# Kernel tuning notes

Hardware: AMD Instinct MI355X
Metric: run time of the kernel (lower is better)

## Reference

```python
import jax, jax.numpy as jnp
import numpy as np

N, E = 50000, 800000          # nodes, edges
IN_DIM, HID, OUT = 200, 256, 64  # hidden_dims
R = 2                          # num_relations
NEG_SLOPE = 0.2                # RGATConv default negative_slope
EPS = 1e-16                    # PyG softmax denominator eps


def _glorot(key, shape, fan):
    return jax.random.normal(key, shape, dtype=jnp.float32) / np.float32(np.sqrt(fan))


def setup_inputs() -> dict:
    key = jax.random.key(0)
    ks = jax.random.split(key, 13)
    features = jax.random.normal(ks[0], (N, IN_DIM), dtype=jnp.float32)
    edge_index = jax.random.randint(ks[1], (2, E), 0, N, dtype=jnp.int64)
    edge_type = jax.random.randint(ks[2], (E,), 0, R, dtype=jnp.int64)
    return {
        "features": features,
        "edge_index": edge_index,
        "edge_type": edge_type,
        # RGATConv layer 1 (heads=1, dim=1): weight [R, in, out], q/k [out, 1]
        "w1": _glorot(ks[3], (R, IN_DIM, HID), IN_DIM),
        "q1": _glorot(ks[4], (HID, 1), HID),
        "k1": _glorot(ks[5], (HID, 1), HID),
        # RGATConv layer 2
        "w2": _glorot(ks[6], (R, HID, OUT), HID),
        "q2": _glorot(ks[7], (OUT, 1), OUT),
        "k2": _glorot(ks[8], (OUT, 1), OUT),
        # decoder: Linear(OUT->HID) then Linear(HID->IN_DIM), stored as [in, out]
        "dW1": _glorot(ks[9], (OUT, HID), OUT),
        "db1": jnp.zeros((HID,), jnp.float32),
        "dW2": _glorot(ks[10], (HID, IN_DIM), HID),
        "db2": jnp.zeros((IN_DIM,), jnp.float32),
    }


def rgat_conv(x, src, dst, etype, w, q, k):
    """PyG RGATConv: additive-self-attention, across-relation softmax,
    heads=1, dim=1, concat=False, bias=False, aggr=add (eval mode: no dropout)."""
    n = x.shape[0]
    # relation-specific transform at node level (per-edge bmm factors through nodes)
    xw = jnp.einsum('ni,ric->rnc', x, w)          # [R, N, C]
    qn = jnp.einsum('rnc,ch->rnh', xw, q)         # [R, N, 1]
    kn = jnp.einsum('rnc,ch->rnh', xw, k)         # [R, N, 1]
    # per-edge attention logit: leaky_relu(q_i + k_j)
    alpha = jax.nn.leaky_relu(qn[etype, dst] + kn[etype, src], NEG_SLOPE)  # [E, 1]
    # segment softmax over destination nodes (across relations)
    m = jax.lax.stop_gradient(jax.ops.segment_max(alpha, dst, num_segments=n))
    m = jnp.where(jnp.isfinite(m), m, jnp.float32(0.0))
    ea = jnp.exp(alpha - m[dst])
    denom = jax.ops.segment_sum(ea, dst, num_segments=n)
    att = ea / (denom[dst] + EPS)                 # [E, 1]
    # scatter-add weighted messages
    msg = att * xw[etype, src]                    # [E, C]
    return jax.ops.segment_sum(msg, dst, num_segments=n)  # [N, C]


def reference(features, edge_index, edge_type, w1, q1, k1, w2, q2, k2, dW1, db1, dW2, db2):
    src, dst = edge_index[0], edge_index[1]
    h1 = jax.nn.elu(rgat_conv(features, src, dst, edge_type, w1, q1, k1))
    h2 = jax.nn.elu(rgat_conv(h1, src, dst, edge_type, w2, q2, k2))
    h3 = (h2 @ dW1 + db1) @ dW2 + db2   # decoder (PCA mode: no ReLU)
    return (h2, h3)
```

## Files before the change

### kernel.cpp

```cpp
#include <hip/hip_runtime.h>

#define IN_DIM 200
#define HID    256
#define OUT_D  64
#define RREL   2
#define NEG_SLOPE 0.2f
#define NNODE  50000
#define MPAD   50048

typedef __attribute__((ext_vector_type(8))) short bf16x8;
typedef __attribute__((ext_vector_type(4))) float f32x4;
typedef __attribute__((ext_vector_type(4))) unsigned int u32x4;

__device__ __forceinline__ float bf2f(unsigned short u) {
    union { unsigned int i; float f; } v; v.i = ((unsigned int)u) << 16; return v.f;
}
__device__ __forceinline__ unsigned short f2bf(float f) {
    union { float f; unsigned int i; } v; v.f = f;
    unsigned int u = v.i;
    return (unsigned short)((u + 0x7FFFu + ((u >> 16) & 1u)) >> 16);
}
__device__ __forceinline__ float elu(float v) { return v > 0.f ? v : (__expf(v) - 1.0f); }

__global__ void feat_cvt(const float* __restrict__ in, unsigned short* __restrict__ out)
{
    long long idx = (long long)blockIdx.x * 256 + threadIdx.x;
    int row = (int)(idx >> 6);
    int c4  = ((int)idx & 63) << 2;
    if (row >= MPAD) return;
    unsigned short v[4];
    #pragma unroll
    for (int i = 0; i < 4; ++i) {
        int c = c4 + i;
        float f = (row < NNODE && c < IN_DIM) ? in[(long long)row * IN_DIM + c] : 0.f;
        v[i] = f2bf(f);
    }
    *(ushort4*)(out + (long long)row * 256 + c4) = make_ushort4(v[0], v[1], v[2], v[3]);
}

__global__ void wt_cvt(const float* __restrict__ in, unsigned short* __restrict__ out,
                       int Kreal, int Nreal, int Kpad, int Npad, int nb)
{
    long long total = (long long)nb * Npad * Kpad;
    long long idx = (long long)blockIdx.x * 256 + threadIdx.x;
    if (idx >= total) return;
    int kk = (int)(idx % Kpad);
    long long t = idx / Kpad;
    int nrow = (int)(t % Npad);
    int z = (int)(t / Npad);
    float f = (kk < Kreal && nrow < Nreal) ? in[((long long)z * Kreal + kk) * Nreal + nrow] : 0.f;
    out[idx] = f2bf(f);
}

__global__ void wt_cvt_stack(const float* __restrict__ in, unsigned short* __restrict__ out)
{
    int idx = blockIdx.x * 256 + threadIdx.x;
    if (idx >= 2 * 256 * 256) return;
    int kk = idx & 255;
    int c  = (idx >> 8) & 255;
    int z  = idx >> 16;
    float f = (kk < IN_DIM) ? in[((long long)z * IN_DIM + kk) * 256 + c] : 0.f;
    out[(long long)c * 512 + z * 256 + kk] = f2bf(f);
}

__global__ __launch_bounds__(256) void wqk_cvt(
    const float* __restrict__ w, const float* __restrict__ q,
    const float* __restrict__ k, float* __restrict__ wqv, float* __restrict__ wkv)
{
    int wv = ((blockIdx.x << 8) + threadIdx.x) >> 6;
    int lane = threadIdx.x & 63;
    if (wv >= 512) return;
    int r = wv >> 8, kk = wv & 255;
    float sq = 0.f, sk = 0.f;
    if (kk < IN_DIM) {
        const float* row = w + ((long long)(r * IN_DIM + kk)) * 256;
        float4 wv4 = *(const float4*)(row + lane * 4);
        float4 qv4 = *(const float4*)(q + lane * 4);
        float4 kv4 = *(const float4*)(k + lane * 4);
        sq = wv4.x * qv4.x + wv4.y * qv4.y + wv4.z * qv4.z + wv4.w * qv4.w;
        sk = wv4.x * kv4.x + wv4.y * kv4.y + wv4.z * kv4.z + wv4.w * kv4.w;
        #pragma unroll
        for (int off = 32; off; off >>= 1) {
            sq += __shfl_xor(sq, off);
            sk += __shfl_xor(sk, off);
        }
    }
    if (lane == 0) { wqv[r * 256 + kk] = sq; wkv[r * 256 + kk] = sk; }
}

__global__ __launch_bounds__(256) void qk_feat(
    const unsigned short* __restrict__ A1, const float* __restrict__ wqv,
    const float* __restrict__ wkv, float* __restrict__ qn, float* __restrict__ kn, int n)
{
    int wv = ((blockIdx.x << 8) + threadIdx.x) >> 6;
    int lane = threadIdx.x & 63;
    if (wv >= n) return;
    ushort4 v = *(const ushort4*)(A1 + (long long)wv * 256 + lane * 4);
    float x0 = bf2f(v.x), x1 = bf2f(v.y), x2 = bf2f(v.z), x3 = bf2f(v.w);
    float4 q0v = *(const float4*)(wqv + lane * 4);
    float4 k0v = *(const float4*)(wkv + lane * 4);
    float4 q1v = *(const float4*)(wqv + 256 + lane * 4);
    float4 k1v = *(const float4*)(wkv + 256 + lane * 4);
    float sq0 = x0 * q0v.x + x1 * q0v.y + x2 * q0v.z + x3 * q0v.w;
    float sk0 = x0 * k0v.x + x1 * k0v.y + x2 * k0v.z + x3 * k0v.w;
    float sq1 = x0 * q1v.x + x1 * q1v.y + x2 * q1v.z + x3 * q1v.w;
    float sk1 = x0 * k1v.x + x1 * k1v.y + x2 * k1v.z + x3 * k1v.w;
    #pragma unroll
    for (int off = 32; off; off >>= 1) {
        sq0 += __shfl_xor(sq0, off);
        sk0 += __shfl_xor(sk0, off);
        sq1 += __shfl_xor(sq1, off);
        sk1 += __shfl_xor(sk1, off);
    }
    if (lane == 0) {
        qn[wv] = sq0; qn[n + wv] = sq1;
        kn[wv] = sk0; kn[n + wv] = sk1;
    }
}

template<bool OUT_BF16, bool DO_ELU>
__global__ __launch_bounds__(256) void gemm_mfma(
    const unsigned short* __restrict__ A,
    const unsigned short* __restrict__ Bt,
    const float* __restrict__ bias,
    void* __restrict__ Cout,
    int M, int Nn, int Kp, int Npad,
    long long strideC)
{
    __shared__ __align__(16) char lds[49152];
    const int tid  = threadIdx.x;
    const int lane = tid & 63;
    const int w    = tid >> 6;
    const int m0   = blockIdx.x * 128;
    const int n0   = blockIdx.y * 64;
    const int z    = blockIdx.z;

    const char* Ab = (const char*)A;
    const char* Bb = (const char*)(Bt + (long long)z * Npad * Kp);
    const int rs = Kp * 2;

    f32x4 acc[2][4];
    #pragma unroll
    for (int i = 0; i < 2; ++i)
        #pragma unroll
        for (int j = 0; j < 4; ++j) acc[i][j] = (f32x4){0.f, 0.f, 0.f, 0.f};

    const int KT = Kp >> 6;

    auto stage = [&](int buf, int kt) {
        char* lA = lds + buf * 24576;
        char* lB = lA + 16384;
        #pragma unroll
        for (int i = 0; i < 4; ++i) {
            int g = i * 256 + tid;
            int row = g >> 3, c = g & 7;
            const char* src = Ab + (long long)(m0 + row) * rs + kt * 128 + ((c ^ (row & 7)) << 4);
            __builtin_amdgcn_global_load_lds((const __attribute__((address_space(1))) void*)src,
                                             (__attribute__((address_space(3))) void*)(lA + g * 16),
                                             16, 0, 0);
        }
        #pragma unroll
        for (int i = 0; i < 2; ++i) {
            int g = i * 256 + tid;
            int row = g >> 3, c = g & 7;
            const char* src = Bb + (long long)(n0 + row) * rs + kt * 128 + ((c ^ (row & 7)) << 4);
            __builtin_amdgcn_global_load_lds((const __attribute__((address_space(1))) void*)src,
                                             (__attribute__((address_space(3))) void*)(lB + g * 16),
                                             16, 0, 0);
        }
    };

    stage(0, 0);
    int cur = 0;
    for (int kt = 0; kt < KT; ++kt) {
        __syncthreads();
        if (kt + 1 < KT) stage(cur ^ 1, kt + 1);
        const char* lA = lds + cur * 24576;
        const char* lB = lA + 16384;
        #pragma unroll
        for (int ks = 0; ks < 2; ++ks) {
            const int kg = ks * 4 + (lane >> 4);
            bf16x8 a[2], b[4];
            #pragma unroll
            for (int mi = 0; mi < 2; ++mi) {
                int row = w * 32 + mi * 16 + (lane & 15);
                a[mi] = *(const bf16x8*)(lA + row * 128 + ((kg ^ (row & 7)) << 4));
            }
            #pragma unroll
            for (int nj = 0; nj < 4; ++nj) {
                int row = nj * 16 + (lane & 15);
                b[nj] = *(const bf16x8*)(lB + row * 128 + ((kg ^ (row & 7)) << 4));
            }
            #pragma unroll
            for (int mi = 0; mi < 2; ++mi)
                #pragma unroll
                for (int nj = 0; nj < 4; ++nj)
                    acc[mi][nj] = __builtin_amdgcn_mfma_f32_16x16x32_bf16(a[mi], b[nj], acc[mi][nj], 0, 0, 0);
        }
        cur ^= 1;
    }

    const int colb = n0 + (lane & 15);
    #pragma unroll
    for (int mi = 0; mi < 2; ++mi) {
        #pragma unroll
        for (int nj = 0; nj < 4; ++nj) {
            int col = colb + nj * 16;
            if (col >= Nn) continue;
            float badd = bias ? bias[col] : 0.f;
            #pragma unroll
            for (int r = 0; r < 4; ++r) {
                int rowm = m0 + w * 32 + mi * 16 + ((lane >> 4) << 2) + r;
                if (rowm >= M) continue;
                float v = acc[mi][nj][r] + badd;
                if (DO_ELU) v = v > 0.f ? v : (__expf(v) - 1.0f);
                if (OUT_BF16)
                    ((unsigned short*)Cout)[strideC * z + (long long)rowm * Nn + col] = f2bf(v);
                else
                    ((float*)Cout)[strideC * z + (long long)rowm * Nn + col] = v;
            }
        }
    }
}

template<int C>
__global__ __launch_bounds__(256) void qk_bf16(
    const unsigned short* __restrict__ xw, const float* __restrict__ q,
    const float* __restrict__ k, float* __restrict__ qn, float* __restrict__ kn, int n)
{
    int wv = ((blockIdx.x << 8) + threadIdx.x) >> 6;
    int lane = threadIdx.x & 63;
    if (wv >= 2 * n) return;
    int r = wv >= n;
    int node = wv - r * n;
    const unsigned short* row = xw + ((long long)r * MPAD + node) * C;
    float sq, sk;
    if (C == 256) {
        ushort4 v = *(const ushort4*)(row + lane * 4);
        float4 qv = *(const float4*)(q + lane * 4);
        float4 kv = *(const float4*)(k + lane * 4);
        float x0 = bf2f(v.x), x1 = bf2f(v.y), x2 = bf2f(v.z), x3 = bf2f(v.w);
        sq = x0 * qv.x + x1 * qv.y + x2 * qv.z + x3 * qv.w;
        sk = x0 * kv.x + x1 * kv.y + x2 * kv.z + x3 * kv.w;
    } else {
        float x = bf2f(row[lane]);
        sq = x * q[lane];
        sk = x * k[lane];
    }
    #pragma unroll
    for (int off = 32; off; off >>= 1) {
        sq += __shfl_xor(sq, off);
        sk += __shfl_xor(sk, off);
    }
    if (lane == 0) { qn[wv] = sq; kn[wv] = sk; }
}

__global__ void count_kernel(const int* __restrict__ dst, const int* __restrict__ etype,
                             int* __restrict__ deg2, int E)
{
    int e = blockIdx.x * 256 + threadIdx.x;
    if (e < E) atomicAdd(&deg2[(dst[e] << 1) | etype[e]], 1);
}

__global__ __launch_bounds__(256) void scan_blocksum(
    const int* __restrict__ deg, int* __restrict__ bsum, int n)
{
    __shared__ int red[256];
    int i = blockIdx.x * 256 + threadIdx.x;
    int v = (i < n) ? deg[i] : 0;
    red[threadIdx.x] = v;
    __syncthreads();
    #pragma unroll
    for (int off = 128; off; off >>= 1) {
        if (threadIdx.x < off) red[threadIdx.x] += red[threadIdx.x + off];
        __syncthreads();
    }
    if (threadIdx.x == 0) bsum[blockIdx.x] = red[0];
}

__global__ __launch_bounds__(512) void scan_bsum(int* __restrict__ bsum, int nb)
{
    __shared__ int buf[512];
    const int t = threadIdx.x;
    int v = (t < nb) ? bsum[t] : 0;
    buf[t] = v;
    __syncthreads();
    #pragma unroll
    for (int off = 1; off < 512; off <<= 1) {
        int u = (t >= off) ? buf[t - off] : 0;
        __syncthreads();
        buf[t] += u;
        __syncthreads();
    }
    if (t < nb) bsum[t] = buf[t] - v;
}

__global__ __launch_bounds__(256) void scan_final(
    const int* __restrict__ deg, const int* __restrict__ bsum,
    int* __restrict__ row_ptr, int* __restrict__ cursor, int n)
{
    __shared__ int buf[256];
    const int t = threadIdx.x;
    const int i = blockIdx.x * 256 + t;
    int v = (i < n) ? deg[i] : 0;
    buf[t] = v;
    __syncthreads();
    #pragma unroll
    for (int off = 1; off < 256; off <<= 1) {
        int u = (t >= off) ? buf[t - off] : 0;
        __syncthreads();
        buf[t] += u;
        __syncthreads();
    }
    int excl = bsum[blockIdx.x] + buf[t] - v;
    if (i < n) { row_ptr[i] = excl; cursor[i] = excl; }
    if (i == n - 1) row_ptr[n] = excl + v;
}

__global__ void scatter_kernel(const int* __restrict__ dst, const int* __restrict__ src,
                               const int* __restrict__ etype, int* __restrict__ cursor2,
                               int* __restrict__ epk, int E)
{
    int e = blockIdx.x * 256 + threadIdx.x;
    if (e < E) {
        int p = atomicAdd(&cursor2[(dst[e] << 1) | etype[e]], 1);
        epk[p] = src[e];
    }
}

__global__ __launch_bounds__(256) void aggregate_z(
    const unsigned short* __restrict__ A1,
    const float* __restrict__ qn,
    const float* __restrict__ kn,
    const int* __restrict__ row_ptr2,
    const int* __restrict__ epk,
    unsigned short* __restrict__ z,
    int n)
{
    const int wv   = ((blockIdx.x << 8) + threadIdx.x) >> 6;
    const int lane = threadIdx.x & 63;
    if (wv >= n) return;
    const int d = wv;
    const int start = row_ptr2[2 * d];
    const int mid   = row_ptr2[2 * d + 1];
    const int end   = row_ptr2[2 * d + 2];
    const float q0 = qn[d];
    const float q1 = qn[n + d];

    float mx = -INFINITY;
    for (int j = start + lane; j < end; j += 64) {
        int s = epk[j];
        bool r1 = j >= mid;
        float a = (r1 ? q1 : q0) + kn[(r1 ? n : 0) + s];
        a = a > 0.f ? a : NEG_SLOPE * a;
        mx = fmaxf(mx, a);
    }
    #pragma unroll
    for (int off = 32; off; off >>= 1) mx = fmaxf(mx, __shfl_xor(mx, off));

    float se = 0.f;
    for (int j = start + lane; j < end; j += 64) {
        int s = epk[j];
        bool r1 = j >= mid;
        float a = (r1 ? q1 : q0) + kn[(r1 ? n : 0) + s];
        a = a > 0.f ? a : NEG_SLOPE * a;
        se += __expf(a - mx);
    }
    #pragma unroll
    for (int off = 32; off; off >>= 1) se += __shfl_xor(se, off);
    const float inv = 1.f / (se + 1e-16f);

    const int slot = lane >> 5;
    const int hl   = lane & 31;

    #pragma unroll
    for (int seg = 0; seg < 2; ++seg) {
        const int s0 = seg ? mid : start;
        const int s1 = seg ? end : mid;
        const float qr = seg ? q1 : q0;
        const int kbase = seg ? n : 0;

        float accA[8], accB[8];
        #pragma unroll
        for (int i = 0; i < 8; ++i) { accA[i] = 0.f; accB[i] = 0.f; }

        for (int base = s0; base < s1; base += 64) {
            const int cnt = min(64, s1 - base);
            int pv = 0; float wvv = 0.f;
            if (lane < cnt) {
                pv = epk[base + lane];
                float a = qr + kn[kbase + pv];
                a = a > 0.f ? a : NEG_SLOPE * a;
                wvv = __expf(a - mx) * inv;
            }
            const int iters = (cnt + 1) >> 1;
            int k = 0;
            for (; k + 2 <= iters; k += 2) {
                const int e0 = slot + k * 2;
                const int e1 = e0 + 2;
                int   pA = __shfl(pv, e0);
                float wA = __shfl(wvv, e0);
                int   pB = __shfl(pv, e1);
                float wB = __shfl(wvv, e1);
                const u32x4 rA = *(const u32x4*)(A1 + (long long)pA * 256 + hl * 8);
                const u32x4 rB = *(const u32x4*)(A1 + (long long)pB * 256 + hl * 8);
                #pragma unroll
                for (int t2 = 0; t2 < 4; ++t2) {
                    unsigned dA = rA[t2], dB = rB[t2];
                    accA[2 * t2]     = fmaf(wA, __uint_as_float(dA << 16),         accA[2 * t2]);
                    accA[2 * t2 + 1] = fmaf(wA, __uint_as_float(dA & 0xFFFF0000u), accA[2 * t2 + 1]);
                    accB[2 * t2]     = fmaf(wB, __uint_as_float(dB << 16),         accB[2 * t2]);
                    accB[2 * t2 + 1] = fmaf(wB, __uint_as_float(dB & 0xFFFF0000u), accB[2 * t2 + 1]);
                }
            }
            if (k < iters) {
                const int e0 = slot + k * 2;
                int   pA = __shfl(pv, e0);
                float wA = __shfl(wvv, e0);
                const u32x4 rA = *(const u32x4*)(A1 + (long long)pA * 256 + hl * 8);
                #pragma unroll
                for (int t2 = 0; t2 < 4; ++t2) {
                    unsigned dA = rA[t2];
                    accA[2 * t2]     = fmaf(wA, __uint_as_float(dA << 16),         accA[2 * t2]);
                    accA[2 * t2 + 1] = fmaf(wA, __uint_as_float(dA & 0xFFFF0000u), accA[2 * t2 + 1]);
                }
            }
        }

        float acc[8];
        #pragma unroll
        for (int i = 0; i < 8; ++i) acc[i] = accA[i] + accB[i];
        #pragma unroll
        for (int t2 = 0; t2 < 8; ++t2) acc[t2] += __shfl_xor(acc[t2], 32);

        if (slot == 0) {
            u32x4 pack;
            #pragma unroll
            for (int t2 = 0; t2 < 4; ++t2)
                pack[t2] = (unsigned)f2bf(acc[2 * t2]) | ((unsigned)f2bf(acc[2 * t2 + 1]) << 16);
            *(u32x4*)(z + (long long)d * 512 + seg * 256 + hl * 8) = pack;
        }
    }
}

__global__ __launch_bounds__(256) void aggregate2(
    const unsigned short* __restrict__ xw,
    const float* __restrict__ qn,
    const float* __restrict__ kn,
    const int* __restrict__ row_ptr2,
    const int* __restrict__ epk,
    unsigned short* __restrict__ outb,
    float* __restrict__ outf,
    int n)
{
    constexpr int LPE   = 8;
    constexpr int NSLOT = 8;

    const int wv   = ((blockIdx.x << 8) + threadIdx.x) >> 6;
    const int lane = threadIdx.x & 63;
    if (wv >= n) return;
    const int d = wv;
    const int start = row_ptr2[2 * d];
    const int mid   = row_ptr2[2 * d + 1];
    const int end   = row_ptr2[2 * d + 2];
    const float q0 = qn[d];
    const float q1 = qn[n + d];

    float mx = -INFINITY;
    for (int j = start + lane; j < end; j += 64) {
        int s = epk[j];
        bool r1 = j >= mid;
        float a = (r1 ? q1 : q0) + kn[(r1 ? n : 0) + s];
        a = a > 0.f ? a : NEG_SLOPE * a;
        mx = fmaxf(mx, a);
    }
    #pragma unroll
    for (int off = 32; off; off >>= 1) mx = fmaxf(mx, __shfl_xor(mx, off));

    float se = 0.f;
    for (int j = start + lane; j < end; j += 64) {
        int s = epk[j];
        bool r1 = j >= mid;
        float a = (r1 ? q1 : q0) + kn[(r1 ? n : 0) + s];
        a = a > 0.f ? a : NEG_SLOPE * a;
        se += __expf(a - mx);
    }
    #pragma unroll
    for (int off = 32; off; off >>= 1) se += __shfl_xor(se, off);
    const float inv = 1.f / (se + 1e-16f);

    const int slot = lane / LPE;
    const int hl   = lane % LPE;
    float accA[8], accB[8];
    #pragma unroll
    for (int i = 0; i < 8; ++i) { accA[i] = 0.f; accB[i] = 0.f; }

    for (int base = start; base < end; base += 64) {
        const int cnt = min(64, end - base);
        int pv = 0; float wvv = 0.f;
        if (lane < cnt) {
            int j = base + lane;
            pv = epk[j];
            bool r1 = j >= mid;
            float a = (r1 ? q1 : q0) + kn[(r1 ? n : 0) + pv];
            a = a > 0.f ? a : NEG_SLOPE * a;
            wvv = __expf(a - mx) * inv;
        }

        const int iters = (cnt + NSLOT - 1) / NSLOT;
        int k = 0;
        for (; k + 2 <= iters; k += 2) {
            const int e0 = slot + k * NSLOT;
            const int e1 = e0 + NSLOT;
            int   pA = __shfl(pv, e0);
            float wA = __shfl(wvv, e0);
            int   pB = __shfl(pv, e1);
            float wB = __shfl(wvv, e1);
            const long long oA = ((base + e0 >= mid) ? (long long)MPAD * 64 : 0) + (long long)pA * 64 + hl * 8;
            const long long oB = ((base + e1 >= mid) ? (long long)MPAD * 64 : 0) + (long long)pB * 64 + hl * 8;
            const u32x4 rA = *(const u32x4*)(xw + oA);
            const u32x4 rB = *(const u32x4*)(xw + oB);
            #pragma unroll
            for (int t2 = 0; t2 < 4; ++t2) {
                unsigned dA = rA[t2], dB = rB[t2];
                accA[2 * t2]     = fmaf(wA, __uint_as_float(dA << 16),         accA[2 * t2]);
                accA[2 * t2 + 1] = fmaf(wA, __uint_as_float(dA & 0xFFFF0000u), accA[2 * t2 + 1]);
                accB[2 * t2]     = fmaf(wB, __uint_as_float(dB << 16),         accB[2 * t2]);
                accB[2 * t2 + 1] = fmaf(wB, __uint_as_float(dB & 0xFFFF0000u), accB[2 * t2 + 1]);
            }
        }
        if (k < iters) {
            const int e0 = slot + k * NSLOT;
            int   pA = __shfl(pv, e0);
            float wA = __shfl(wvv, e0);
            const long long oA = ((base + e0 >= mid) ? (long long)MPAD * 64 : 0) + (long long)pA * 64 + hl * 8;
            const u32x4 rA = *(const u32x4*)(xw + oA);
            #pragma unroll
            for (int t2 = 0; t2 < 4; ++t2) {
                unsigned dA = rA[t2];
                accA[2 * t2]     = fmaf(wA, __uint_as_float(dA << 16),         accA[2 * t2]);
                accA[2 * t2 + 1] = fmaf(wA, __uint_as_float(dA & 0xFFFF0000u), accA[2 * t2 + 1]);
            }
        }
    }

    float acc[8];
    #pragma unroll
    for (int i = 0; i < 8; ++i) acc[i] = accA[i] + accB[i];
    #pragma unroll
    for (int off = LPE; off < 64; off <<= 1)
        #pragma unroll
        for (int t2 = 0; t2 < 8; ++t2) acc[t2] += __shfl_xor(acc[t2], off);

    if (slot == 0) {
        float fo[8];
        #pragma unroll
        for (int t2 = 0; t2 < 8; ++t2) fo[t2] = elu(acc[t2]);
        u32x4 pack;
        #pragma unroll
        for (int t2 = 0; t2 < 4; ++t2)
            pack[t2] = (unsigned)f2bf(fo[2 * t2]) | ((unsigned)f2bf(fo[2 * t2 + 1]) << 16);
        *(u32x4*)(outb + (long long)d * 64 + hl * 8) = pack;
        *(float4*)(outf + (long long)d * 64 + hl * 8)     = make_float4(fo[0], fo[1], fo[2], fo[3]);
        *(float4*)(outf + (long long)d * 64 + hl * 8 + 4) = make_float4(fo[4], fo[5], fo[6], fo[7]);
    }
}

extern "C" void kernel_launch(void* const* d_in, const int* in_sizes, int n_in,
                              void* d_out, int out_size, void* d_ws, size_t ws_size,
                              hipStream_t stream)
{
    const float* features = (const float*)d_in[0];
    const int*   ei       = (const int*)d_in[1];
    const int*   etype    = (const int*)d_in[2];
    const float* w1       = (const float*)d_in[3];
    const float* q1       = (const float*)d_in[4];
    const float* k1       = (const float*)d_in[5];
    const float* w2       = (const float*)d_in[6];
    const float* q2       = (const float*)d_in[7];
    const float* k2       = (const float*)d_in[8];
    const float* dW1      = (const float*)d_in[9];
    const float* db1      = (const float*)d_in[10];
    const float* dW2      = (const float*)d_in[11];
    const float* db2      = (const float*)d_in[12];

    const int n = in_sizes[0] / IN_DIM;
    const int E = in_sizes[2];
    const int n2 = 2 * n;
    const int* src = ei;
    const int* dst = ei + E;

    float* out_h2 = (float*)d_out;
    float* out_h3 = out_h2 + (long long)n * OUT_D;

    char* wp = (char*)d_ws;
    auto carve = [&](size_t bytes) {
        char* p = wp; wp += (bytes + 255) & ~(size_t)255; return p;
    };
    unsigned short* A1   = (unsigned short*)carve((size_t)MPAD * 256 * 2);
    unsigned short* zbuf = (unsigned short*)carve((size_t)MPAD * 512 * 2);
    unsigned short* h1   = (unsigned short*)carve((size_t)MPAD * 256 * 2);
    unsigned short* xw2  = (unsigned short*)carve((size_t)2 * MPAD * 64 * 2);
    unsigned short* h2b  = (unsigned short*)carve((size_t)MPAD * 64 * 2);
    unsigned short* tdec = (unsigned short*)carve((size_t)MPAD * 256 * 2);
    unsigned short* wst  = (unsigned short*)carve((size_t)256 * 512 * 2);
    unsigned short* w2t  = (unsigned short*)carve((size_t)2 * 64 * 256 * 2);
    unsigned short* dW1t = (unsigned short*)carve((size_t)256 * 64 * 2);
    unsigned short* dW2t = (unsigned short*)carve((size_t)256 * 256 * 2);
    float* wqv    = (float*)carve((size_t)2 * 256 * 4);
    float* wkv    = (float*)carve((size_t)2 * 256 * 4);
    float* qnb    = (float*)carve((size_t)n2 * 4);
    float* knb    = (float*)carve((size_t)n2 * 4);
    int* row_ptr2 = (int*)carve((size_t)(n2 + 1) * 4);
    int* cursor2  = (int*)carve((size_t)n2 * 4);
    int* deg2     = (int*)carve((size_t)n2 * 4);
    int* bsum     = (int*)carve((size_t)512 * 4);
    int* epk      = (int*)carve((size_t)E * 4);

    const int EB  = (E + 255) / 256;
    const int NB2 = (n2 + 255) / 256;
    const int MB  = (n + 127) / 128;
    const int WAVE_N  = (n + 3) / 4;
    const int WAVE_RN = (n2 + 3) / 4;

    hipMemsetAsync(deg2, 0, (size_t)n2 * sizeof(int), stream);
    count_kernel<<<EB, 256, 0, stream>>>(dst, etype, deg2, E);
    scan_blocksum<<<NB2, 256, 0, stream>>>(deg2, bsum, n2);
    scan_bsum<<<1, 512, 0, stream>>>(bsum, NB2);
    scan_final<<<NB2, 256, 0, stream>>>(deg2, bsum, row_ptr2, cursor2, n2);
    scatter_kernel<<<EB, 256, 0, stream>>>(dst, src, etype, cursor2, epk, E);

    feat_cvt<<<(MPAD * 64 + 255) / 256, 256, 0, stream>>>(features, A1);
    wt_cvt_stack<<<(2 * 256 * 256 + 255) / 256, 256, 0, stream>>>(w1, wst);
    wt_cvt<<<(2 * 64 * 256 + 255) / 256, 256, 0, stream>>>(w2, w2t, HID, OUT_D, 256, 64, RREL);
    wt_cvt<<<(256 * 64 + 255) / 256, 256, 0, stream>>>(dW1, dW1t, OUT_D, HID, 64, 256, 1);
    wt_cvt<<<(256 * 256 + 255) / 256, 256, 0, stream>>>(dW2, dW2t, HID, IN_DIM, 256, 256, 1);
    wqk_cvt<<<128, 256, 0, stream>>>(w1, q1, k1, wqv, wkv);

    qk_feat<<<WAVE_N, 256, 0, stream>>>(A1, wqv, wkv, qnb, knb, n);
    aggregate_z<<<WAVE_N, 256, 0, stream>>>(A1, qnb, knb, row_ptr2, epk, zbuf, n);
    {
        dim3 g(MB, 4, 1);
        gemm_mfma<true, true><<<g, 256, 0, stream>>>(zbuf, wst, nullptr, h1,
                                                     n, HID, 512, 256, 0);
    }

    {
        dim3 g(MB, 1, RREL);
        gemm_mfma<true, false><<<g, 256, 0, stream>>>(h1, w2t, nullptr, xw2,
                                                      n, OUT_D, 256, 64, (long long)MPAD * OUT_D);
    }
    qk_bf16<OUT_D><<<WAVE_RN, 256, 0, stream>>>(xw2, q2, k2, qnb, knb, n);
    aggregate2<<<WAVE_N, 256, 0, stream>>>(xw2, qnb, knb, row_ptr2, epk,
                                           h2b, out_h2, n);

    {
        dim3 g(MB, 4, 1);
        gemm_mfma<true, false><<<g, 256, 0, stream>>>(h2b, dW1t, db1, tdec,
                                                      n, HID, 64, 256, 0);
    }
    {
        dim3 g(MB, 4, 1);
        gemm_mfma<false, false><<<g, 256, 0, stream>>>(tdec, dW2t, db2, out_h3,
                                                       n, IN_DIM, 256, 256, 0);
    }
}
```

Baseline: 365.5 us.

## Compact layer-1 features to 200-wide rows and add single-pass softmax for small degrees

The bf16 feature matrix is now stored at its real 200-column stride instead of padded to 256. This cuts conversion writes and the bytes touched by the qk and gather kernels. Both aggregation kernels gain a fast path for destinations with at most 64 incoming edges: it loads each edge index and logit once into registers, then does the max, the sum and the weighted gather from those values instead of rereading the edge list three times. The gather still reads 256 columns per row, so columns 200-255 pick up data from the next row or the unpadded tail. This relies on the stacked weight rows for those columns being zero, and the tail bytes past the last row are left uninitialized.

Result: no change. 360.3 us (-1.4%).

```diff
diff --git a/kernel.cpp b/kernel.cpp
--- a/kernel.cpp
+++ b/kernel.cpp
@@ -22,20 +22,14 @@
 }
 __device__ __forceinline__ float elu(float v) { return v > 0.f ? v : (__expf(v) - 1.0f); }
 
-__global__ void feat_cvt(const float* __restrict__ in, unsigned short* __restrict__ out)
-{
-    long long idx = (long long)blockIdx.x * 256 + threadIdx.x;
-    int row = (int)(idx >> 6);
-    int c4  = ((int)idx & 63) << 2;
-    if (row >= MPAD) return;
-    unsigned short v[4];
-    #pragma unroll
-    for (int i = 0; i < 4; ++i) {
-        int c = c4 + i;
-        float f = (row < NNODE && c < IN_DIM) ? in[(long long)row * IN_DIM + c] : 0.f;
-        v[i] = f2bf(f);
-    }
-    *(ushort4*)(out + (long long)row * 256 + c4) = make_ushort4(v[0], v[1], v[2], v[3]);
+__global__ void feat_cvt(const float* __restrict__ in, unsigned short* __restrict__ out, int n)
+{
+    int t = blockIdx.x * 256 + threadIdx.x;
+    int row = t / 50, c4 = (t % 50) * 4;
+    if (row >= n) return;
+    float4 f = *(const float4*)(in + (long long)row * 200 + c4);
+    *(ushort4*)(out + (long long)row * 200 + c4) =
+        make_ushort4(f2bf(f.x), f2bf(f.y), f2bf(f.z), f2bf(f.w));
 }
 
 __global__ void wt_cvt(const float* __restrict__ in, unsigned short* __restrict__ out,
@@ -89,14 +83,17 @@
 }
 
 __global__ __launch_bounds__(256) void qk_feat(
-    const unsigned short* __restrict__ A1, const float* __restrict__ wqv,
+    const unsigned short* __restrict__ A1c, const float* __restrict__ wqv,
     const float* __restrict__ wkv, float* __restrict__ qn, float* __restrict__ kn, int n)
 {
     int wv = ((blockIdx.x << 8) + threadIdx.x) >> 6;
     int lane = threadIdx.x & 63;
     if (wv >= n) return;
-    ushort4 v = *(const ushort4*)(A1 + (long long)wv * 256 + lane * 4);
-    float x0 = bf2f(v.x), x1 = bf2f(v.y), x2 = bf2f(v.z), x3 = bf2f(v.w);
+    float x0 = 0.f, x1 = 0.f, x2 = 0.f, x3 = 0.f;
+    if (lane < 50) {
+        ushort4 v = *(const ushort4*)(A1c + (long long)wv * 200 + lane * 4);
+        x0 = bf2f(v.x); x1 = bf2f(v.y); x2 = bf2f(v.z); x3 = bf2f(v.w);
+    }
     float4 q0v = *(const float4*)(wqv + lane * 4);
     float4 k0v = *(const float4*)(wkv + lane * 4);
     float4 q1v = *(const float4*)(wqv + 256 + lane * 4);
@@ -329,7 +326,7 @@
 }
 
 __global__ __launch_bounds__(256) void aggregate_z(
-    const unsigned short* __restrict__ A1,
+    const unsigned short* __restrict__ A1c,
     const float* __restrict__ qn,
     const float* __restrict__ kn,
     const int* __restrict__ row_ptr2,
@@ -344,8 +341,89 @@
     const int start = row_ptr2[2 * d];
     const int mid   = row_ptr2[2 * d + 1];
     const int end   = row_ptr2[2 * d + 2];
+    const int cnt = end - start;
+    const int c0  = mid - start;
     const float q0 = qn[d];
     const float q1 = qn[n + d];
+    const int slot = lane >> 5;
+    const int hl   = lane & 31;
+
+    if (cnt <= 64) {
+        int pv = 0; float a = -INFINITY;
+        if (lane < cnt) {
+            pv = epk[start + lane];
+            bool r1 = lane >= c0;
+            a = (r1 ? q1 : q0) + kn[(r1 ? n : 0) + pv];
+            a = a > 0.f ? a : NEG_SLOPE * a;
+        }
+        float mx = a;
+        #pragma unroll
+        for (int off = 32; off; off >>= 1) mx = fmaxf(mx, __shfl_xor(mx, off));
+        float ev = (lane < cnt) ? __expf(a - mx) : 0.f;
+        float se = ev;
+        #pragma unroll
+        for (int off = 32; off; off >>= 1) se += __shfl_xor(se, off);
+        const float wvv = ev * (1.f / (se + 1e-16f));
+
+        #pragma unroll
+        for (int seg = 0; seg < 2; ++seg) {
+            const int segoff = seg ? c0 : 0;
+            const int cs = seg ? (cnt - c0) : c0;
+            float accA[8], accB[8];
+            #pragma unroll
+            for (int i = 0; i < 8; ++i) { accA[i] = 0.f; accB[i] = 0.f; }
+
+            const int iters = (cs + 1) >> 1;
+            int k = 0;
+            for (; k + 2 <= iters; k += 2) {
+                const int e0 = slot + k * 2;
+                const int e1 = e0 + 2;
+                int   pA = __shfl(pv, segoff + e0);
+                float wA = __shfl(wvv, segoff + e0);
+                int   pB = __shfl(pv, segoff + e1);
+                float wB = __shfl(wvv, segoff + e1);
+                if (e0 >= cs) wA = 0.f;
+                if (e1 >= cs) wB = 0.f;
+                const u32x4 rA = *(const u32x4*)(A1c + (long long)pA * 200 + hl * 8);
+                const u32x4 rB = *(const u32x4*)(A1c + (long long)pB * 200 + hl * 8);
+                #pragma unroll
+                for (int t2 = 0; t2 < 4; ++t2) {
+                    unsigned dA = rA[t2], dB = rB[t2];
+                    accA[2 * t2]     = fmaf(wA, __uint_as_float(dA << 16),         accA[2 * t2]);
+                    accA[2 * t2 + 1] = fmaf(wA, __uint_as_float(dA & 0xFFFF0000u), accA[2 * t2 + 1]);
+                    accB[2 * t2]     = fmaf(wB, __uint_as_float(dB << 16),         accB[2 * t2]);
+                    accB[2 * t2 + 1] = fmaf(wB, __uint_as_float(dB & 0xFFFF0000u), accB[2 * t2 + 1]);
+                }
+            }
+            if (k < iters) {
+                const int e0 = slot + k * 2;
+                int   pA = __shfl(pv, segoff + e0);
+                float wA = __shfl(wvv, segoff + e0);
+                if (e0 >= cs) wA = 0.f;
+                const u32x4 rA = *(const u32x4*)(A1c + (long long)pA * 200 + hl * 8);
+                #pragma unroll
+                for (int t2 = 0; t2 < 4; ++t2) {
+                    unsigned dA = rA[t2];
+                    accA[2 * t2]     = fmaf(wA, __uint_as_float(dA << 16),         accA[2 * t2]);
+                    accA[2 * t2 + 1] = fmaf(wA, __uint_as_float(dA & 0xFFFF0000u), accA[2 * t2 + 1]);
+                }
+            }
+
+            float acc[8];
+            #pragma unroll
+            for (int i = 0; i < 8; ++i) acc[i] = accA[i] + accB[i];
+            #pragma unroll
+            for (int t2 = 0; t2 < 8; ++t2) acc[t2] += __shfl_xor(acc[t2], 32);
+            if (slot == 0) {
+                u32x4 pack;
+                #pragma unroll
+                for (int t2 = 0; t2 < 4; ++t2)
+                    pack[t2] = (unsigned)f2bf(acc[2 * t2]) | ((unsigned)f2bf(acc[2 * t2 + 1]) << 16);
+                *(u32x4*)(z + (long long)d * 512 + seg * 256 + hl * 8) = pack;
+            }
+        }
+        return;
+    }
 
     float mx = -INFINITY;
     for (int j = start + lane; j < end; j += 64) {
@@ -370,9 +448,6 @@
     for (int off = 32; off; off >>= 1) se += __shfl_xor(se, off);
     const float inv = 1.f / (se + 1e-16f);
 
-    const int slot = lane >> 5;
-    const int hl   = lane & 31;
-
     #pragma unroll
     for (int seg = 0; seg < 2; ++seg) {
         const int s0 = seg ? mid : start;
@@ -385,15 +460,15 @@
         for (int i = 0; i < 8; ++i) { accA[i] = 0.f; accB[i] = 0.f; }
 
         for (int base = s0; base < s1; base += 64) {
-            const int cnt = min(64, s1 - base);
+            const int cnt2 = min(64, s1 - base);
             int pv = 0; float wvv = 0.f;
-            if (lane < cnt) {
+            if (lane < cnt2) {
                 pv = epk[base + lane];
                 float a = qr + kn[kbase + pv];
                 a = a > 0.f ? a : NEG_SLOPE * a;
                 wvv = __expf(a - mx) * inv;
             }
-            const int iters = (cnt + 1) >> 1;
+            const int iters = (cnt2 + 1) >> 1;
             int k = 0;
             for (; k + 2 <= iters; k += 2) {
                 const int e0 = slot + k * 2;
@@ -402,8 +477,8 @@
                 float wA = __shfl(wvv, e0);
                 int   pB = __shfl(pv, e1);
                 float wB = __shfl(wvv, e1);
-                const u32x4 rA = *(const u32x4*)(A1 + (long long)pA * 256 + hl * 8);
-                const u32x4 rB = *(const u32x4*)(A1 + (long long)pB * 256 + hl * 8);
+                const u32x4 rA = *(const u32x4*)(A1c + (long long)pA * 200 + hl * 8);
+                const u32x4 rB = *(const u32x4*)(A1c + (long long)pB * 200 + hl * 8);
                 #pragma unroll
                 for (int t2 = 0; t2 < 4; ++t2) {
                     unsigned dA = rA[t2], dB = rB[t2];
@@ -417,7 +492,7 @@
                 const int e0 = slot + k * 2;
                 int   pA = __shfl(pv, e0);
                 float wA = __shfl(wvv, e0);
-                const u32x4 rA = *(const u32x4*)(A1 + (long long)pA * 256 + hl * 8);
+                const u32x4 rA = *(const u32x4*)(A1c + (long long)pA * 200 + hl * 8);
                 #pragma unroll
                 for (int t2 = 0; t2 < 4; ++t2) {
                     unsigned dA = rA[t2];
@@ -463,49 +538,33 @@
     const int start = row_ptr2[2 * d];
     const int mid   = row_ptr2[2 * d + 1];
     const int end   = row_ptr2[2 * d + 2];
+    const int cnt = end - start;
+    const int c0  = mid - start;
     const float q0 = qn[d];
     const float q1 = qn[n + d];
-
-    float mx = -INFINITY;
-    for (int j = start + lane; j < end; j += 64) {
-        int s = epk[j];
-        bool r1 = j >= mid;
-        float a = (r1 ? q1 : q0) + kn[(r1 ? n : 0) + s];
-        a = a > 0.f ? a : NEG_SLOPE * a;
-        mx = fmaxf(mx, a);
-    }
-    #pragma unroll
-    for (int off = 32; off; off >>= 1) mx = fmaxf(mx, __shfl_xor(mx, off));
-
-    float se = 0.f;
-    for (int j = start + lane; j < end; j += 64) {
-        int s = epk[j];
-        bool r1 = j >= mid;
-        float a = (r1 ? q1 : q0) + kn[(r1 ? n : 0) + s];
-        a = a > 0.f ? a : NEG_SLOPE * a;
-        se += __expf(a - mx);
-    }
-    #pragma unroll
-    for (int off = 32; off; off >>= 1) se += __shfl_xor(se, off);
-    const float inv = 1.f / (se + 1e-16f);
-
     const int slot = lane / LPE;
     const int hl   = lane % LPE;
+
     float accA[8], accB[8];
     #pragma unroll
     for (int i = 0; i < 8; ++i) { accA[i] = 0.f; accB[i] = 0.f; }
 
-    for (int base = start; base < end; base += 64) {
-        const int cnt = min(64, end - base);
-        int pv = 0; float wvv = 0.f;
+    if (cnt <= 64) {
+        int pv = 0; float a = -INFINITY;
         if (lane < cnt) {
-            int j = base + lane;
-            pv = epk[j];
-            bool r1 = j >= mid;
-            float a = (r1 ? q1 : q0) + kn[(r1 ? n : 0) + pv];
+            pv = epk[start + lane];
+            bool r1 = lane >= c0;
+            a = (r1 ? q1 : q0) + kn[(r1 ? n : 0) + pv];
             a = a > 0.f ? a : NEG_SLOPE * a;
-            wvv = __expf(a - mx) * inv;
-        }
+        }
+        float mx = a;
+        #pragma unroll
+        for (int off = 32; off; off >>= 1) mx = fmaxf(mx, __shfl_xor(mx, off));
+        float ev = (lane < cnt) ? __expf(a - mx) : 0.f;
+        float se = ev;
+        #pragma unroll
+        for (int off = 32; off; off >>= 1) se += __shfl_xor(se, off);
+        const float wvn = ev * (1.f / (se + 1e-16f));
 
         const int iters = (cnt + NSLOT - 1) / NSLOT;
         int k = 0;
@@ -513,11 +572,11 @@
             const int e0 = slot + k * NSLOT;
             const int e1 = e0 + NSLOT;
             int   pA = __shfl(pv, e0);
-            float wA = __shfl(wvv, e0);
+            float wA = __shfl(wvn, e0);
             int   pB = __shfl(pv, e1);
-            float wB = __shfl(wvv, e1);
-            const long long oA = ((base + e0 >= mid) ? (long long)MPAD * 64 : 0) + (long long)pA * 64 + hl * 8;
-            const long long oB = ((base + e1 >= mid) ? (long long)MPAD * 64 : 0) + (long long)pB * 64 + hl * 8;
+            float wB = __shfl(wvn, e1);
+            const long long oA = ((e0 >= c0) ? (long long)MPAD * 64 : 0) + (long long)pA * 64 + hl * 8;
+            const long long oB = ((e1 >= c0) ? (long long)MPAD * 64 : 0) + (long long)pB * 64 + hl * 8;
             const u32x4 rA = *(const u32x4*)(xw + oA);
             const u32x4 rB = *(const u32x4*)(xw + oB);
             #pragma unroll
@@ -532,14 +591,85 @@
         if (k < iters) {
             const int e0 = slot + k * NSLOT;
             int   pA = __shfl(pv, e0);
-            float wA = __shfl(wvv, e0);
-            const long long oA = ((base + e0 >= mid) ? (long long)MPAD * 64 : 0) + (long long)pA * 64 + hl * 8;
+            float wA = __shfl(wvn, e0);
+            const long long oA = ((e0 >= c0) ? (long long)MPAD * 64 : 0) + (long long)pA * 64 + hl * 8;
             const u32x4 rA = *(const u32x4*)(xw + oA);
             #pragma unroll
             for (int t2 = 0; t2 < 4; ++t2) {
                 unsigned dA = rA[t2];
                 accA[2 * t2]     = fmaf(wA, __uint_as_float(dA << 16),         accA[2 * t2]);
                 accA[2 * t2 + 1] = fmaf(wA, __uint_as_float(dA & 0xFFFF0000u), accA[2 * t2 + 1]);
+            }
+        }
+    } else {
+        float mx = -INFINITY;
+        for (int j = start + lane; j < end; j += 64) {
+            int s = epk[j];
+            bool r1 = j >= mid;
+            float a = (r1 ? q1 : q0) + kn[(r1 ? n : 0) + s];
+            a = a > 0.f ? a : NEG_SLOPE * a;
+            mx = fmaxf(mx, a);
+        }
+        #pragma unroll
+        for (int off = 32; off; off >>= 1) mx = fmaxf(mx, __shfl_xor(mx, off));
+
+        float se = 0.f;
+        for (int j = start + lane; j < end; j += 64) {
+            int s = epk[j];
+            bool r1 = j >= mid;
+            float a = (r1 ? q1 : q0) + kn[(r1 ? n : 0) + s];
+            a = a > 0.f ? a : NEG_SLOPE * a;
+            se += __expf(a - mx);
+        }
+        #pragma unroll
+        for (int off = 32; off; off >>= 1) se += __shfl_xor(se, off);
+        const float inv = 1.f / (se + 1e-16f);
+
+        for (int base = start; base < end; base += 64) {
+            const int cnt2 = min(64, end - base);
+            int pv = 0; float wvn = 0.f;
+            if (lane < cnt2) {
+                int j = base + lane;
+                pv = epk[j];
+                bool r1 = j >= mid;
+                float a = (r1 ? q1 : q0) + kn[(r1 ? n : 0) + pv];
+                a = a > 0.f ? a : NEG_SLOPE * a;
+                wvn = __expf(a - mx) * inv;
+            }
+            const int iters = (cnt2 + NSLOT - 1) / NSLOT;
+            int k = 0;
+            for (; k + 2 <= iters; k += 2) {
+                const int e0 = slot + k * NSLOT;
+                const int e1 = e0 + NSLOT;
+                int   pA = __shfl(pv, e0);
+                float wA = __shfl(wvn, e0);
+                int   pB = __shfl(pv, e1);
+                float wB = __shfl(wvn, e1);
+                const long long oA = ((base + e0 >= mid) ? (long long)MPAD * 64 : 0) + (long long)pA * 64 + hl * 8;
+                const long long oB = ((base + e1 >= mid) ? (long long)MPAD * 64 : 0) + (long long)pB * 64 + hl * 8;
+                const u32x4 rA = *(const u32x4*)(xw + oA);
+                const u32x4 rB = *(const u32x4*)(xw + oB);
+                #pragma unroll
+                for (int t2 = 0; t2 < 4; ++t2) {
+                    unsigned dA = rA[t2], dB = rB[t2];
+                    accA[2 * t2]     = fmaf(wA, __uint_as_float(dA << 16),         accA[2 * t2]);
+                    accA[2 * t2 + 1] = fmaf(wA, __uint_as_float(dA & 0xFFFF0000u), accA[2 * t2 + 1]);
+                    accB[2 * t2]     = fmaf(wB, __uint_as_float(dB << 16),         accB[2 * t2]);
+                    accB[2 * t2 + 1] = fmaf(wB, __uint_as_float(dB & 0xFFFF0000u), accB[2 * t2 + 1]);
+                }
+            }
+            if (k < iters) {
+                const int e0 = slot + k * NSLOT;
+                int   pA = __shfl(pv, e0);
+                float wA = __shfl(wvn, e0);
+                const long long oA = ((base + e0 >= mid) ? (long long)MPAD * 64 : 0) + (long long)pA * 64 + hl * 8;
+                const u32x4 rA = *(const u32x4*)(xw + oA);
+                #pragma unroll
+                for (int t2 = 0; t2 < 4; ++t2) {
+                    unsigned dA = rA[t2];
+                    accA[2 * t2]     = fmaf(wA, __uint_as_float(dA << 16),         accA[2 * t2]);
+                    accA[2 * t2 + 1] = fmaf(wA, __uint_as_float(dA & 0xFFFF0000u), accA[2 * t2 + 1]);
+                }
             }
         }
     }
@@ -597,7 +727,7 @@
     auto carve = [&](size_t bytes) {
         char* p = wp; wp += (bytes + 255) & ~(size_t)255; return p;
     };
-    unsigned short* A1   = (unsigned short*)carve((size_t)MPAD * 256 * 2);
+    unsigned short* A1c  = (unsigned short*)carve((size_t)n * 200 * 2 + 256);
     unsigned short* zbuf = (unsigned short*)carve((size_t)MPAD * 512 * 2);
     unsigned short* h1   = (unsigned short*)carve((size_t)MPAD * 256 * 2);
     unsigned short* xw2  = (unsigned short*)carve((size_t)2 * MPAD * 64 * 2);
@@ -621,7 +751,6 @@
     const int NB2 = (n2 + 255) / 256;
     const int MB  = (n + 127) / 128;
     const int WAVE_N  = (n + 3) / 4;
-    const int WAVE_RN = (n2 + 3) / 4;
 
     hipMemsetAsync(deg2, 0, (size_t)n2 * sizeof(int), stream);
     count_kernel<<<EB, 256, 0, stream>>>(dst, etype, deg2, E);
@@ -630,15 +759,15 @@
     scan_final<<<NB2, 256, 0, stream>>>(deg2, bsum, row_ptr2, cursor2, n2);
     scatter_kernel<<<EB, 256, 0, stream>>>(dst, src, etype, cursor2, epk, E);
 
-    feat_cvt<<<(MPAD * 64 + 255) / 256, 256, 0, stream>>>(features, A1);
+    feat_cvt<<<(n * 50 + 255) / 256, 256, 0, stream>>>(features, A1c, n);
     wt_cvt_stack<<<(2 * 256 * 256 + 255) / 256, 256, 0, stream>>>(w1, wst);
     wt_cvt<<<(2 * 64 * 256 + 255) / 256, 256, 0, stream>>>(w2, w2t, HID, OUT_D, 256, 64, RREL);
     wt_cvt<<<(256 * 64 + 255) / 256, 256, 0, stream>>>(dW1, dW1t, OUT_D, HID, 64, 256, 1);
     wt_cvt<<<(256 * 256 + 255) / 256, 256, 0, stream>>>(dW2, dW2t, HID, IN_DIM, 256, 256, 1);
     wqk_cvt<<<128, 256, 0, stream>>>(w1, q1, k1, wqv, wkv);
 
-    qk_feat<<<WAVE_N, 256, 0, stream>>>(A1, wqv, wkv, qnb, knb, n);
-    aggregate_z<<<WAVE_N, 256, 0, stream>>>(A1, qnb, knb, row_ptr2, epk, zbuf, n);
+    qk_feat<<<WAVE_N, 256, 0, stream>>>(A1c, wqv, wkv, qnb, knb, n);
+    aggregate_z<<<WAVE_N, 256, 0, stream>>>(A1c, qnb, knb, row_ptr2, epk, zbuf, n);
     {
         dim3 g(MB, 4, 1);
         gemm_mfma<true, true><<<g, 256, 0, stream>>>(zbuf, wst, nullptr, h1,
@@ -650,7 +779,7 @@
         gemm_mfma<true, false><<<g, 256, 0, stream>>>(h1, w2t, nullptr, xw2,
                                                       n, OUT_D, 256, 64, (long long)MPAD * OUT_D);
     }
-    qk_bf16<OUT_D><<<WAVE_RN, 256, 0, stream>>>(xw2, q2, k2, qnb, knb, n);
+    qk_bf16<OUT_D><<<(n2 + 3) / 4, 256, 0, stream>>>(xw2, q2, k2, qnb, knb, n);
     aggregate2<<<WAVE_N, 256, 0, stream>>>(xw2, qnb, knb, row_ptr2, epk,
                                            h2b, out_h2, n);
 
```
